# Kernel optimization log

Hardware: AMD Instinct MI355X
Metric: run time of the kernel (lower is better)

The kernel has to match this reference:

```python
import math
import jax, jax.numpy as jnp
import numpy as np

N_BLOCKS = 8
D_MODEL = 1024
D_FF = 4096
B, T = 4, 2048
EPS = 1e-5


def setup_inputs() -> dict:
    key = jax.random.key(0)
    ks = jax.random.split(key, 8)
    s = 0.02  # small init so deep stack stays numerically sane
    return {
        "x": jax.random.normal(ks[0], (B, T, D_MODEL), jnp.float32),
        "ln1_w": jnp.ones((N_BLOCKS, D_MODEL), jnp.float32),
        "ln1_b": jnp.zeros((N_BLOCKS, D_MODEL), jnp.float32),
        "qkv_w": jax.random.normal(ks[1], (N_BLOCKS, 3 * D_MODEL, D_MODEL), jnp.float32) * s,
        "qkv_b": jnp.zeros((N_BLOCKS, 3 * D_MODEL), jnp.float32),
        "out_w": jax.random.normal(ks[2], (N_BLOCKS, D_MODEL, D_MODEL), jnp.float32) * s,
        "out_b": jnp.zeros((N_BLOCKS, D_MODEL), jnp.float32),
        "ln2_w": jnp.ones((N_BLOCKS, D_MODEL), jnp.float32),
        "ln2_b": jnp.zeros((N_BLOCKS, D_MODEL), jnp.float32),
        "ff0_w": jax.random.normal(ks[3], (N_BLOCKS, D_FF, D_MODEL), jnp.float32) * s,
        "ff0_b": jnp.zeros((N_BLOCKS, D_FF), jnp.float32),
        "ff3_w": jax.random.normal(ks[4], (N_BLOCKS, D_MODEL, D_FF), jnp.float32) * s,
        "ff3_b": jnp.zeros((N_BLOCKS, D_MODEL), jnp.float32),
    }


def _layer_norm(x, w, b):
    mean = jnp.mean(x, axis=-1, keepdims=True)
    var = jnp.mean(jnp.square(x - mean), axis=-1, keepdims=True)
    return (x - mean) / jnp.sqrt(var + EPS) * w + b


def reference(x, ln1_w, ln1_b, qkv_w, qkv_b, out_w, out_b,
              ln2_w, ln2_b, ff0_w, ff0_b, ff3_w, ff3_b):
    Bq, Tq, C = x.shape
    scale = 1.0 / math.sqrt(C)
    mask = jnp.triu(jnp.ones((Tq, Tq), bool), k=1)  # True above diagonal -> masked

    def block(xc, p):
        l1w, l1b, qw, qb, ow, ob, l2w, l2b, f0w, f0b, f3w, f3b = p
        h = _layer_norm(xc, l1w, l1b)
        qkv = h @ qw.T + qb  # [B,T,3C]
        q, k, v = jnp.split(qkv, 3, axis=-1)
        att = jnp.einsum('btc,bsc->bts', q, k) * scale
        att = jnp.where(mask, -jnp.inf, att)
        att = jax.nn.softmax(att, axis=-1)
        out = jnp.einsum('bts,bsc->btc', att, v)
        xc = xc + out @ ow.T + ob
        h2 = _layer_norm(xc, l2w, l2b)
        ff = jax.nn.gelu(h2 @ f0w.T + f0b, approximate=False)
        xc = xc + ff @ f3w.T + f3b
        return xc, None

    params = (ln1_w, ln1_b, qkv_w, qkv_b, out_w, out_b,
              ln2_w, ln2_b, ff0_w, ff0_b, ff3_w, ff3_b)
    x, _ = jax.lax.scan(block, x, params)
    return x
```

## Files before the change

### kernel.cpp

```cpp
#include <hip/hip_runtime.h>
#include <hip/hip_bf16.h>
#include <math.h>


typedef __bf16 bf16;
typedef __bf16 bf16x8 __attribute__((ext_vector_type(8)));
typedef __bf16 bf16x4 __attribute__((ext_vector_type(4)));
typedef float f32x4 __attribute__((ext_vector_type(4)));

#define BM 128
#define BN 128
#define BK 32

__device__ __forceinline__ void async_load16(const void* g, void* l) {
  __builtin_amdgcn_global_load_lds(
      (const __attribute__((address_space(1))) void*)g,
      (__attribute__((address_space(3))) void*)l, 16, 0, 0);
}

constexpr int EPI_BF16 = 0;
constexpr int EPI_GELU = 1;
constexpr int EPI_RESID = 2;
constexpr int EPI_F32SCALE = 3;

template <int EPI>
__global__ __launch_bounds__(256, 4) void gemm_bt(
    const bf16* __restrict__ A, const bf16* __restrict__ Bw,
    const float* __restrict__ bias, const float* __restrict__ resid,
    void* __restrict__ Cout, int K, int lda, int ldb, int ldc,
    long batchA, long batchB, long batchC, float alpha,
    int causalSkip, int kLimit) {
  const int nx = gridDim.x;
  const int lin = blockIdx.y * nx + blockIdx.x;
  const int xcd = lin & 7;
  const int t = lin >> 3;
  const int n_idx = t % nx;
  const int j_idx = t / nx;
  const int m0 = (xcd + 8 * j_idx) * BM;
  const int n0 = n_idx * BN;
  if (causalSkip && n0 > m0) return;
  const int bz = blockIdx.z;
  const bf16* Ab = A + (long)bz * batchA;
  const bf16* Bb = Bw + (long)bz * batchB;
  const int kEnd = kLimit ? ((m0 + BM < K) ? (m0 + BM) : K) : K;

  __shared__ bf16 As[BM * BK];
  __shared__ bf16 Bs[BN * BK];

  const int tid = threadIdx.x;
  const int wave = tid >> 6;
  const int lane = tid & 63;
  const int wr = wave >> 1;
  const int wc = wave & 1;
  const int l16 = lane & 15;
  const int kq = lane >> 4;

  const bf16* gAp[2];
  const bf16* gBp[2];
  bf16* lAp[2];
  bf16* lBp[2];
#pragma unroll
  for (int rep = 0; rep < 2; rep++) {
    const int c = tid + rep * 256;
    const int r = c >> 2;
    const int qc = (c & 3) ^ ((r >> 1) & 3);
    gAp[rep] = Ab + (long)(m0 + r) * lda + qc * 8;
    gBp[rep] = Bb + (long)(n0 + r) * ldb + qc * 8;
    lAp[rep] = As + (c & ~63) * 8;
    lBp[rep] = Bs + (c & ~63) * 8;
  }

  const int swz = (l16 >> 1) & 3;
  const int kqs = (kq ^ swz) * 8;
  int offA[4], offB[4];
#pragma unroll
  for (int i = 0; i < 4; i++) {
    offA[i] = (wr * 64 + i * 16 + l16) * BK + kqs;
    offB[i] = (wc * 64 + i * 16 + l16) * BK + kqs;
  }

  f32x4 acc[4][4] = {};

  for (int k0 = 0; k0 < kEnd; k0 += BK) {
#pragma unroll
    for (int rep = 0; rep < 2; rep++) {
      async_load16(gAp[rep], lAp[rep]);
      async_load16(gBp[rep], lBp[rep]);
      gAp[rep] += BK;
      gBp[rep] += BK;
    }
    __syncthreads();
    bf16x8 af[4], bfr[4];
#pragma unroll
    for (int i = 0; i < 4; i++) af[i] = *(const bf16x8*)(As + offA[i]);
#pragma unroll
    for (int j = 0; j < 4; j++) bfr[j] = *(const bf16x8*)(Bs + offB[j]);
#pragma unroll
    for (int i = 0; i < 4; i++)
#pragma unroll
      for (int j = 0; j < 4; j++)
        acc[i][j] = __builtin_amdgcn_mfma_f32_16x16x32_bf16(af[i], bfr[j],
                                                            acc[i][j], 0, 0, 0);
    __syncthreads();
  }

  const int baseRow = m0 + wr * 64 + (lane >> 4) * 4;
  const int baseCol = n0 + wc * 64 + l16;
#pragma unroll
  for (int j = 0; j < 4; j++) {
    const int col = baseCol + j * 16;
    float bv = 0.0f;
    if (EPI != EPI_F32SCALE && bias != nullptr) bv = bias[col];
#pragma unroll
    for (int i = 0; i < 4; i++) {
      const int row0 = baseRow + i * 16;
#pragma unroll
      for (int r = 0; r < 4; r++) {
        const float v = acc[i][j][r];
        const long idx = (long)bz * batchC + (long)(row0 + r) * ldc + col;
        if (EPI == EPI_F32SCALE) {
          ((float*)Cout)[idx] = v * alpha;
        } else if (EPI == EPI_RESID) {
          ((float*)Cout)[idx] = resid[idx] + v + bv;
        } else if (EPI == EPI_GELU) {
          const float u = v + bv;
          const float g = 0.5f * u * (1.0f + erff(u * 0.70710678118654752f));
          ((bf16*)Cout)[idx] = (bf16)g;
        } else {
          ((bf16*)Cout)[idx] = (bf16)(v + bv);
        }
      }
    }
  }
}

__global__ __launch_bounds__(256) void ln_kernel(
    const float* __restrict__ x, const float* __restrict__ w,
    const float* __restrict__ b, bf16* __restrict__ out) {
  const int C = 1024;
  const long row = blockIdx.x;
  const int t = threadIdx.x;
  const float4 v = ((const float4*)(x + row * C))[t];
  float s = v.x + v.y + v.z + v.w;
  float sq = v.x * v.x + v.y * v.y + v.z * v.z + v.w * v.w;
#pragma unroll
  for (int o = 1; o < 64; o <<= 1) {
    s += __shfl_xor(s, o, 64);
    sq += __shfl_xor(sq, o, 64);
  }
  __shared__ float rs[4], rq[4];
  const int wv = t >> 6, ln = t & 63;
  if (!ln) { rs[wv] = s; rq[wv] = sq; }
  __syncthreads();
  s = rs[0] + rs[1] + rs[2] + rs[3];
  sq = rq[0] + rq[1] + rq[2] + rq[3];
  const float mean = s * (1.0f / 1024.0f);
  const float var = sq * (1.0f / 1024.0f) - mean * mean;
  const float rstd = rsqrtf(var + 1e-5f);
  const float4 wv4 = ((const float4*)w)[t];
  const float4 bv4 = ((const float4*)b)[t];
  bf16x4 o = {(bf16)((v.x - mean) * rstd * wv4.x + bv4.x),
              (bf16)((v.y - mean) * rstd * wv4.y + bv4.y),
              (bf16)((v.z - mean) * rstd * wv4.z + bv4.z),
              (bf16)((v.w - mean) * rstd * wv4.w + bv4.w)};
  ((bf16x4*)(out + row * C))[t] = o;
}

__global__ __launch_bounds__(256) void softmax_causal(
    const float* __restrict__ S, bf16* __restrict__ P) {
  const int T = 2048;
  const int t = blockIdx.x, b = blockIdx.y;
  const long rowoff = ((long)b * T + t) * (long)T;
  const float* row = S + rowoff;
  bf16* prow = P + rowoff;
  const int L = t + 1;
  const int tid = threadIdx.x;
  float vals[8];
  float mx = -1e30f;
#pragma unroll
  for (int i = 0; i < 8; i++) {
    const int idx = tid + i * 256;
    if (idx < L) {
      vals[i] = row[idx];
      mx = fmaxf(mx, vals[i]);
    } else {
      vals[i] = -1e30f;
    }
  }
#pragma unroll
  for (int o = 1; o < 64; o <<= 1) mx = fmaxf(mx, __shfl_xor(mx, o, 64));
  __shared__ float red[4], red2[4];
  const int wv = tid >> 6, ln = tid & 63;
  if (!ln) red[wv] = mx;
  __syncthreads();
  mx = fmaxf(fmaxf(red[0], red[1]), fmaxf(red[2], red[3]));
  float sum = 0.0f;
#pragma unroll
  for (int i = 0; i < 8; i++) {
    const int idx = tid + i * 256;
    const float e = (idx < L) ? __expf(vals[i] - mx) : 0.0f;
    vals[i] = e;
    sum += e;
  }
#pragma unroll
  for (int o = 1; o < 64; o <<= 1) sum += __shfl_xor(sum, o, 64);
  if (!ln) red2[wv] = sum;
  __syncthreads();
  sum = red2[0] + red2[1] + red2[2] + red2[3];
  const float inv = 1.0f / sum;
#pragma unroll
  for (int i = 0; i < 8; i++) prow[tid + i * 256] = (bf16)(vals[i] * inv);
}

__global__ __launch_bounds__(256) void transpose_v(
    const bf16* __restrict__ qkv, bf16* __restrict__ vt) {
  const int T = 2048, C3 = 3072, C = 1024, COFF = 2048;
  __shared__ bf16 tile[32][33];
  const int b = blockIdx.z;
  const int s0 = blockIdx.x * 32, c0 = blockIdx.y * 32;
  const int tx = threadIdx.x & 31, ty0 = threadIdx.x >> 5;
#pragma unroll
  for (int j = 0; j < 4; j++) {
    const int ty = ty0 + j * 8;
    tile[ty][tx] = qkv[((long)b * T + s0 + ty) * C3 + COFF + c0 + tx];
  }
  __syncthreads();
#pragma unroll
  for (int j = 0; j < 4; j++) {
    const int ty = ty0 + j * 8;
    vt[(long)b * C * T + (long)(c0 + ty) * T + s0 + tx] = tile[tx][ty];
  }
}

__global__ void f2bf_kernel(const float* __restrict__ in,
                            bf16* __restrict__ out, long n4) {
  const long i = (long)blockIdx.x * blockDim.x + threadIdx.x;
  if (i < n4) {
    const float4 v = ((const float4*)in)[i];
    bf16x4 o = {(bf16)v.x, (bf16)v.y, (bf16)v.z, (bf16)v.w};
    ((bf16x4*)out)[i] = o;
  }
}

extern "C" void kernel_launch(void* const* d_in, const int* in_sizes, int n_in,
                              void* d_out, int out_size, void* d_ws,
                              size_t ws_size, hipStream_t stream) {
  const int Bb = 4, T = 2048, C = 1024, FF = 4096, NB = 8;
  const int M = Bb * T;
  const float* x_in = (const float*)d_in[0];
  const float* ln1_w = (const float*)d_in[1];
  const float* ln1_b = (const float*)d_in[2];
  const float* qkv_w = (const float*)d_in[3];
  const float* qkv_b = (const float*)d_in[4];
  const float* out_w = (const float*)d_in[5];
  const float* out_b = (const float*)d_in[6];
  const float* ln2_w = (const float*)d_in[7];
  const float* ln2_b = (const float*)d_in[8];
  const float* ff0_w = (const float*)d_in[9];
  const float* ff0_b = (const float*)d_in[10];
  const float* ff3_w = (const float*)d_in[11];
  const float* ff3_b = (const float*)d_in[12];
  float* x = (float*)d_out;

  char* p = (char*)d_ws;
  auto alloc = [&](size_t bytes) {
    char* r = p;
    p += (bytes + 255) & ~(size_t)255;
    return r;
  };
  bf16* wqkv = (bf16*)alloc((size_t)NB * 3 * C * C * 2);
  bf16* wout = (bf16*)alloc((size_t)NB * C * C * 2);
  bf16* wff0 = (bf16*)alloc((size_t)NB * FF * C * 2);
  bf16* wff3 = (bf16*)alloc((size_t)NB * C * FF * 2);
  bf16* hbuf = (bf16*)alloc((size_t)M * C * 2);
  bf16* qkvb = (bf16*)alloc((size_t)M * 3 * C * 2);
  float* att = (float*)alloc((size_t)Bb * T * T * 4);
  bf16* pbuf = (bf16*)alloc((size_t)Bb * T * T * 2);
  bf16* vt = (bf16*)alloc((size_t)Bb * C * T * 2);
  bf16* aout = (bf16*)alloc((size_t)M * C * 2);
  bf16* ffb = (bf16*)att;

  auto conv = [&](const float* src, bf16* dst, long n) {
    const long n4 = n / 4;
    f2bf_kernel<<<dim3((unsigned)((n4 + 255) / 256)), dim3(256), 0, stream>>>(
        src, dst, n4);
  };
  conv(qkv_w, wqkv, (long)NB * 3 * C * C);
  conv(out_w, wout, (long)NB * C * C);
  conv(ff0_w, wff0, (long)NB * FF * C);
  conv(ff3_w, wff3, (long)NB * C * FF);

  hipMemcpyAsync(x, x_in, (size_t)M * C * 4, hipMemcpyDeviceToDevice, stream);

  const float scale = 1.0f / 32.0f;

  for (int blk = 0; blk < NB; blk++) {
    const bf16* wq = wqkv + (long)blk * 3 * C * C;
    const bf16* wo = wout + (long)blk * C * C;
    const bf16* w0 = wff0 + (long)blk * FF * C;
    const bf16* w3 = wff3 + (long)blk * C * FF;
    const float* l1w = ln1_w + blk * C;
    const float* l1b = ln1_b + blk * C;
    const float* l2w = ln2_w + blk * C;
    const float* l2b = ln2_b + blk * C;
    const float* qb = qkv_b + blk * 3 * C;
    const float* ob = out_b + blk * C;
    const float* f0b = ff0_b + blk * FF;
    const float* f3b = ff3_b + blk * C;

    ln_kernel<<<dim3(M), dim3(256), 0, stream>>>(x, l1w, l1b, hbuf);
    gemm_bt<EPI_BF16><<<dim3(3 * C / BN, M / BM), dim3(256), 0, stream>>>(
        hbuf, wq, qb, nullptr, qkvb, C, C, C, 3 * C, 0, 0, 0, 1.0f, 0, 0);
    gemm_bt<EPI_F32SCALE><<<dim3(T / BN, T / BM, Bb), dim3(256), 0, stream>>>(
        qkvb, qkvb + C, nullptr, nullptr, att, C, 3 * C, 3 * C, T,
        (long)T * 3 * C, (long)T * 3 * C, (long)T * T, scale, 1, 0);
    softmax_causal<<<dim3(T, Bb), dim3(256), 0, stream>>>(att, pbuf);
    transpose_v<<<dim3(T / 32, C / 32, Bb), dim3(256), 0, stream>>>(qkvb, vt);
    gemm_bt<EPI_BF16><<<dim3(C / BN, T / BM, Bb), dim3(256), 0, stream>>>(
        pbuf, vt, nullptr, nullptr, aout, T, T, T, C, (long)T * T, (long)C * T,
        (long)T * C, 1.0f, 0, 1);
    gemm_bt<EPI_RESID><<<dim3(C / BN, M / BM), dim3(256), 0, stream>>>(
        aout, wo, ob, x, x, C, C, C, C, 0, 0, 0, 1.0f, 0, 0);
    ln_kernel<<<dim3(M), dim3(256), 0, stream>>>(x, l2w, l2b, hbuf);
    gemm_bt<EPI_GELU><<<dim3(FF / BN, M / BM), dim3(256), 0, stream>>>(
        hbuf, w0, f0b, nullptr, ffb, C, C, C, FF, 0, 0, 0, 1.0f, 0, 0);
    gemm_bt<EPI_RESID><<<dim3(C / BN, M / BM), dim3(256), 0, stream>>>(
        ffb, w3, f3b, x, x, FF, FF, FF, C, 0, 0, 0, 1.0f, 0, 0);
  }
}
```

Before: 4.047 ms.

## Use 256x256x64 double-buffered GEMM tiles with interleaved async prefetch and MFMA quadrants

Result: slower. 4.383 ms (+8.3%).

```diff
diff --git a/kernel.cpp b/kernel.cpp
--- a/kernel.cpp
+++ b/kernel.cpp
@@ -8,9 +8,9 @@
 typedef __bf16 bf16x4 __attribute__((ext_vector_type(4)));
 typedef float f32x4 __attribute__((ext_vector_type(4)));
 
-#define BM 128
-#define BN 128
-#define BK 32
+#define BM 256
+#define BN 256
+#define BK 64
 
 __device__ __forceinline__ void async_load16(const void* g, void* l) {
   __builtin_amdgcn_global_load_lds(
@@ -18,13 +18,26 @@
       (__attribute__((address_space(3))) void*)l, 16, 0, 0);
 }
 
+__device__ __forceinline__ void barrier_fence() {
+  asm volatile("" ::: "memory");
+  __builtin_amdgcn_s_barrier();
+  asm volatile("" ::: "memory");
+}
+
 constexpr int EPI_BF16 = 0;
 constexpr int EPI_GELU = 1;
 constexpr int EPI_RESID = 2;
 constexpr int EPI_F32SCALE = 3;
 
+#define STAGE(S0, S1, LB, HH, JJ, LD)                                \
+  do {                                                               \
+    const long soff_ = (long)(HH)*128 * (LD) + (long)(JJ)*64;        \
+    async_load16((S0) + soff_, (LB) + (HH)*8192);                    \
+    async_load16((S1) + soff_, (LB) + (HH)*8192 + 4096);             \
+  } while (0)
+
 template <int EPI>
-__global__ __launch_bounds__(256, 4) void gemm_bt(
+__global__ __launch_bounds__(512, 2) void gemm_bt(
     const bf16* __restrict__ A, const bf16* __restrict__ Bw,
     const float* __restrict__ bias, const float* __restrict__ resid,
     void* __restrict__ Cout, int K, int lda, int ldb, int ldc,
@@ -33,9 +46,9 @@
   const int nx = gridDim.x;
   const int lin = blockIdx.y * nx + blockIdx.x;
   const int xcd = lin & 7;
-  const int t = lin >> 3;
-  const int n_idx = t % nx;
-  const int j_idx = t / nx;
+  const int tt = lin >> 3;
+  const int n_idx = tt % nx;
+  const int j_idx = tt / nx;
   const int m0 = (xcd + 8 * j_idx) * BM;
   const int n0 = n_idx * BN;
   if (causalSkip && n0 > m0) return;
@@ -43,81 +56,150 @@
   const bf16* Ab = A + (long)bz * batchA;
   const bf16* Bb = Bw + (long)bz * batchB;
   const int kEnd = kLimit ? ((m0 + BM < K) ? (m0 + BM) : K) : K;
-
-  __shared__ bf16 As[BM * BK];
-  __shared__ bf16 Bs[BN * BK];
+  const int nT = kEnd >> 6;
+
+  __shared__ alignas(16) bf16 sm[65536];
 
   const int tid = threadIdx.x;
   const int wave = tid >> 6;
   const int lane = tid & 63;
-  const int wr = wave >> 1;
-  const int wc = wave & 1;
+  const int wr = wave >> 2;
+  const int wc = wave & 3;
   const int l16 = lane & 15;
   const int kq = lane >> 4;
 
-  const bf16* gAp[2];
-  const bf16* gBp[2];
-  bf16* lAp[2];
-  bf16* lBp[2];
-#pragma unroll
-  for (int rep = 0; rep < 2; rep++) {
-    const int c = tid + rep * 256;
-    const int r = c >> 2;
-    const int qc = (c & 3) ^ ((r >> 1) & 3);
-    gAp[rep] = Ab + (long)(m0 + r) * lda + qc * 8;
-    gBp[rep] = Bb + (long)(n0 + r) * ldb + qc * 8;
-    lAp[rep] = As + (c & ~63) * 8;
-    lBp[rep] = Bs + (c & ~63) * 8;
-  }
-
-  const int swz = (l16 >> 1) & 3;
-  const int kqs = (kq ^ swz) * 8;
-  int offA[4], offB[4];
-#pragma unroll
-  for (int i = 0; i < 4; i++) {
-    offA[i] = (wr * 64 + i * 16 + l16) * BK + kqs;
-    offB[i] = (wc * 64 + i * 16 + l16) * BK + kqs;
-  }
-
-  f32x4 acc[4][4] = {};
-
-  for (int k0 = 0; k0 < kEnd; k0 += BK) {
-#pragma unroll
-    for (int rep = 0; rep < 2; rep++) {
-      async_load16(gAp[rep], lAp[rep]);
-      async_load16(gBp[rep], lBp[rep]);
-      gAp[rep] += BK;
-      gBp[rep] += BK;
+  const int row0 = tid >> 3;
+  const int q0 = (tid & 7) ^ ((tid >> 3) & 7);
+  const bf16* aS0 = Ab + (long)(m0 + row0) * lda + q0 * 8;
+  const bf16* aS1 = aS0 + (long)64 * lda;
+  const bf16* bS0 = Bb + (long)(n0 + row0) * ldb + q0 * 8;
+  const bf16* bS1 = bS0 + (long)64 * ldb;
+  bf16* ldsA = sm + wave * 512;
+  bf16* ldsB = sm + 16384 + wave * 512;
+
+  int xk[2];
+  xk[0] = ((0 + kq) ^ (l16 & 7)) * 8;
+  xk[1] = ((4 + kq) ^ (l16 & 7)) * 8;
+  const int aBase = wr * 8192 + l16 * 64;
+  const int bBase = 16384 + (wc >> 1) * 8192 + (wc & 1) * 4096 + l16 * 64;
+
+  f32x4 acc[8][4] = {};
+  bf16x8 a0[4][2], a1[4][2], b01[2][2], b23[2][2];
+
+  STAGE(aS0, aS1, ldsA, 0, 0, lda);
+  STAGE(aS0, aS1, ldsA, 1, 0, lda);
+  STAGE(bS0, bS1, ldsB, 0, 0, ldb);
+  STAGE(bS0, bS1, ldsB, 1, 0, ldb);
+  STAGE(aS0, aS1, ldsA + 32768, 0, 1, lda);
+  STAGE(aS0, aS1, ldsA + 32768, 1, 1, lda);
+  asm volatile("s_waitcnt vmcnt(4)" ::: "memory");
+  barrier_fence();
+
+  for (int t = 0; t < nT; ++t) {
+    const int b = t & 1;
+    const int aOff = b * 32768 + aBase;
+    const int bOff = b * 32768 + bBase;
+    bf16* sBn = ldsB + (b ^ 1) * 32768;
+    bf16* sAc = ldsA + b * 32768;
+
+#pragma unroll
+    for (int mi = 0; mi < 4; ++mi)
+#pragma unroll
+      for (int ks = 0; ks < 2; ++ks)
+        a0[mi][ks] = *(const bf16x8*)(sm + aOff + mi * 1024 + xk[ks]);
+#pragma unroll
+    for (int ni = 0; ni < 2; ++ni)
+#pragma unroll
+      for (int ks = 0; ks < 2; ++ks)
+        b01[ni][ks] = *(const bf16x8*)(sm + bOff + ni * 1024 + xk[ks]);
+    if (t + 1 < nT) STAGE(bS0, bS1, sBn, 0, t + 1, ldb);
+    barrier_fence();
+    asm volatile("s_waitcnt lgkmcnt(0)" ::: "memory");
+    __builtin_amdgcn_s_setprio(1);
+#pragma unroll
+    for (int mi = 0; mi < 4; ++mi)
+#pragma unroll
+      for (int ni = 0; ni < 2; ++ni)
+#pragma unroll
+        for (int ks = 0; ks < 2; ++ks)
+          acc[mi][ni] = __builtin_amdgcn_mfma_f32_16x16x32_bf16(
+              a0[mi][ks], b01[ni][ks], acc[mi][ni], 0, 0, 0);
+    __builtin_amdgcn_s_setprio(0);
+    barrier_fence();
+
+#pragma unroll
+    for (int mi = 0; mi < 4; ++mi)
+#pragma unroll
+      for (int ks = 0; ks < 2; ++ks)
+        a1[mi][ks] = *(const bf16x8*)(sm + aOff + (mi + 4) * 1024 + xk[ks]);
+#pragma unroll
+    for (int ni = 0; ni < 2; ++ni)
+#pragma unroll
+      for (int ks = 0; ks < 2; ++ks)
+        b23[ni][ks] = *(const bf16x8*)(sm + bOff + (ni + 2) * 1024 + xk[ks]);
+    if (t + 1 < nT) STAGE(bS0, bS1, sBn, 1, t + 1, ldb);
+    barrier_fence();
+    asm volatile("s_waitcnt lgkmcnt(0)" ::: "memory");
+    __builtin_amdgcn_s_setprio(1);
+#pragma unroll
+    for (int mi = 0; mi < 4; ++mi)
+#pragma unroll
+      for (int ni = 0; ni < 2; ++ni)
+#pragma unroll
+        for (int ks = 0; ks < 2; ++ks)
+          acc[mi][ni + 2] = __builtin_amdgcn_mfma_f32_16x16x32_bf16(
+              a0[mi][ks], b23[ni][ks], acc[mi][ni + 2], 0, 0, 0);
+    __builtin_amdgcn_s_setprio(0);
+    barrier_fence();
+
+    if (t + 2 < nT) STAGE(aS0, aS1, sAc, 0, t + 2, lda);
+    barrier_fence();
+    __builtin_amdgcn_s_setprio(1);
+#pragma unroll
+    for (int mi = 0; mi < 4; ++mi)
+#pragma unroll
+      for (int ni = 0; ni < 2; ++ni)
+#pragma unroll
+        for (int ks = 0; ks < 2; ++ks)
+          acc[mi + 4][ni + 2] = __builtin_amdgcn_mfma_f32_16x16x32_bf16(
+              a1[mi][ks], b23[ni][ks], acc[mi + 4][ni + 2], 0, 0, 0);
+    __builtin_amdgcn_s_setprio(0);
+    barrier_fence();
+
+    if (t + 2 < nT) {
+      STAGE(aS0, aS1, sAc, 1, t + 2, lda);
+      asm volatile("s_waitcnt vmcnt(4)" ::: "memory");
+    } else if (t + 1 < nT) {
+      asm volatile("s_waitcnt vmcnt(0)" ::: "memory");
     }
-    __syncthreads();
-    bf16x8 af[4], bfr[4];
-#pragma unroll
-    for (int i = 0; i < 4; i++) af[i] = *(const bf16x8*)(As + offA[i]);
-#pragma unroll
-    for (int j = 0; j < 4; j++) bfr[j] = *(const bf16x8*)(Bs + offB[j]);
-#pragma unroll
-    for (int i = 0; i < 4; i++)
-#pragma unroll
-      for (int j = 0; j < 4; j++)
-        acc[i][j] = __builtin_amdgcn_mfma_f32_16x16x32_bf16(af[i], bfr[j],
-                                                            acc[i][j], 0, 0, 0);
-    __syncthreads();
-  }
-
-  const int baseRow = m0 + wr * 64 + (lane >> 4) * 4;
+    barrier_fence();
+    __builtin_amdgcn_s_setprio(1);
+#pragma unroll
+    for (int mi = 0; mi < 4; ++mi)
+#pragma unroll
+      for (int ni = 0; ni < 2; ++ni)
+#pragma unroll
+        for (int ks = 0; ks < 2; ++ks)
+          acc[mi + 4][ni] = __builtin_amdgcn_mfma_f32_16x16x32_bf16(
+              a1[mi][ks], b01[ni][ks], acc[mi + 4][ni], 0, 0, 0);
+    __builtin_amdgcn_s_setprio(0);
+    barrier_fence();
+  }
+
+  const int baseRow = m0 + wr * 128 + (lane >> 4) * 4;
   const int baseCol = n0 + wc * 64 + l16;
 #pragma unroll
-  for (int j = 0; j < 4; j++) {
-    const int col = baseCol + j * 16;
+  for (int ni = 0; ni < 4; ++ni) {
+    const int col = baseCol + ni * 16;
     float bv = 0.0f;
     if (EPI != EPI_F32SCALE && bias != nullptr) bv = bias[col];
 #pragma unroll
-    for (int i = 0; i < 4; i++) {
-      const int row0 = baseRow + i * 16;
-#pragma unroll
-      for (int r = 0; r < 4; r++) {
-        const float v = acc[i][j][r];
-        const long idx = (long)bz * batchC + (long)(row0 + r) * ldc + col;
+    for (int mi = 0; mi < 8; ++mi) {
+      const int rowb = baseRow + mi * 16;
+#pragma unroll
+      for (int r = 0; r < 4; ++r) {
+        const float v = acc[mi][ni][r];
+        const long idx = (long)bz * batchC + (long)(rowb + r) * ldc + col;
         if (EPI == EPI_F32SCALE) {
           ((float*)Cout)[idx] = v * alpha;
         } else if (EPI == EPI_RESID) {
@@ -309,22 +391,22 @@
     const float* f3b = ff3_b + blk * C;
 
     ln_kernel<<<dim3(M), dim3(256), 0, stream>>>(x, l1w, l1b, hbuf);
-    gemm_bt<EPI_BF16><<<dim3(3 * C / BN, M / BM), dim3(256), 0, stream>>>(
+    gemm_bt<EPI_BF16><<<dim3(3 * C / BN, M / BM), dim3(512), 0, stream>>>(
         hbuf, wq, qb, nullptr, qkvb, C, C, C, 3 * C, 0, 0, 0, 1.0f, 0, 0);
-    gemm_bt<EPI_F32SCALE><<<dim3(T / BN, T / BM, Bb), dim3(256), 0, stream>>>(
+    gemm_bt<EPI_F32SCALE><<<dim3(T / BN, T / BM, Bb), dim3(512), 0, stream>>>(
         qkvb, qkvb + C, nullptr, nullptr, att, C, 3 * C, 3 * C, T,
         (long)T * 3 * C, (long)T * 3 * C, (long)T * T, scale, 1, 0);
     softmax_causal<<<dim3(T, Bb), dim3(256), 0, stream>>>(att, pbuf);
     transpose_v<<<dim3(T / 32, C / 32, Bb), dim3(256), 0, stream>>>(qkvb, vt);
-    gemm_bt<EPI_BF16><<<dim3(C / BN, T / BM, Bb), dim3(256), 0, stream>>>(
+    gemm_bt<EPI_BF16><<<dim3(C / BN, T / BM, Bb), dim3(512), 0, stream>>>(
         pbuf, vt, nullptr, nullptr, aout, T, T, T, C, (long)T * T, (long)C * T,
         (long)T * C, 1.0f, 0, 1);
-    gemm_bt<EPI_RESID><<<dim3(C / BN, M / BM), dim3(256), 0, stream>>>(
+    gemm_bt<EPI_RESID><<<dim3(C / BN, M / BM), dim3(512), 0, stream>>>(
         aout, wo, ob, x, x, C, C, C, C, 0, 0, 0, 1.0f, 0, 0);
     ln_kernel<<<dim3(M), dim3(256), 0, stream>>>(x, l2w, l2b, hbuf);
-    gemm_bt<EPI_GELU><<<dim3(FF / BN, M / BM), dim3(256), 0, stream>>>(
+    gemm_bt<EPI_GELU><<<dim3(FF / BN, M / BM), dim3(512), 0, stream>>>(
         hbuf, w0, f0b, nullptr, ffb, C, C, C, FF, 0, 0, 0, 1.0f, 0, 0);
-    gemm_bt<EPI_RESID><<<dim3(C / BN, M / BM), dim3(256), 0, stream>>>(
+    gemm_bt<EPI_RESID><<<dim3(C / BN, M / BM), dim3(512), 0, stream>>>(
         ffb, w3, f3b, x, x, FF, FF, FF, C, 0, 0, 0, 1.0f, 0, 0);
   }
 }
```
